# Performance work log

Hardware: AMD Instinct MI355X
Metric: run time of the kernel (lower is better)

Reference implementation:

```python
import jax, jax.numpy as jnp
import numpy as np

S, B, C = 7, 2, 20
LAMBDA_COORD, LAMBDA_NOOBJ = 5.0, 0.5
N, T = 16384, 32


def setup_inputs() -> dict:
    key = jax.random.key(0)
    k1, k2, k3 = jax.random.split(key, 3)
    outputs = jax.random.normal(k1, (N, S, S, B * 5 + C), dtype=jnp.float32)
    # center-format normalized boxes [x, y, w, h] in (0, 1)
    target_boxes = jax.random.uniform(k2, (N, T, 4), dtype=jnp.float32)
    target_labels = jax.random.randint(k3, (N, T), 0, C, dtype=jnp.int32)
    return {"outputs": outputs, "target_boxes": target_boxes, "target_labels": target_labels}


def _iou(b1, b2):
    # center-format boxes [..., 4] -> IoU, broadcasting over leading dims
    x11, y11 = b1[..., 0] - b1[..., 2] / 2, b1[..., 1] - b1[..., 3] / 2
    x12, y12 = b1[..., 0] + b1[..., 2] / 2, b1[..., 1] + b1[..., 3] / 2
    x21, y21 = b2[..., 0] - b2[..., 2] / 2, b2[..., 1] - b2[..., 3] / 2
    x22, y22 = b2[..., 0] + b2[..., 2] / 2, b2[..., 1] + b2[..., 3] / 2
    iw = jnp.clip(jnp.minimum(x12, x22) - jnp.maximum(x11, x21), 0.0)
    ih = jnp.clip(jnp.minimum(y12, y22) - jnp.maximum(y11, y21), 0.0)
    inter = iw * ih
    union = b1[..., 2] * b1[..., 3] + b2[..., 2] * b2[..., 3] - inter
    return inter / jnp.maximum(union, 1e-6)


def yolo_v1_loss(outputs, target_boxes, target_labels):
    n = outputs.shape[0]
    pred_boxes = outputs[..., : B * 4].reshape(n, S, S, B, 4)  # [n,S,S,B,4]
    pred_conf = outputs[..., B * 4 : B * 5]                    # [n,S,S,B]
    pred_cls = outputs[..., B * 5 :]                           # [n,S,S,C]

    cell = 1.0 / S
    g = jnp.arange(S, dtype=jnp.float32)
    px = (pred_boxes[..., 0] + g[None, None, :, None]) * cell  # grid_x varies along dim 2
    py = (pred_boxes[..., 1] + g[None, :, None, None]) * cell  # grid_y varies along dim 1
    pred_boxes_g = jnp.stack([px, py, pred_boxes[..., 2], pred_boxes[..., 3]], axis=-1)

    tx, ty, tw, th = (target_boxes[..., i] for i in range(4))
    gxi = jnp.clip((tx / cell).astype(jnp.int32), 0, S - 1)   # [n,T]
    gyi = jnp.clip((ty / cell).astype(jnp.int32), 0, S - 1)
    ox = (tx - gxi.astype(jnp.float32) * cell) / cell
    oy = (ty - gyi.astype(jnp.float32) * cell) / cell

    bidx = jnp.arange(n)[:, None]
    cell_boxes = pred_boxes_g[bidx, gyi, gxi]  # [n,T,B,4]
    cell_conf = pred_conf[bidx, gyi, gxi]      # [n,T,B]
    cell_cls = pred_cls[bidx, gyi, gxi]        # [n,T,C]

    ious = _iou(target_boxes[:, :, None, :], cell_boxes)          # [n,T,B]
    best = jnp.argmax(ious, axis=-1)                              # [n,T]
    best_box = jnp.take_along_axis(cell_boxes, best[..., None, None], axis=2)[:, :, 0]  # [n,T,4]
    best_conf = jnp.take_along_axis(cell_conf, best[..., None], axis=2)[:, :, 0]        # [n,T]

    pw = jnp.maximum(best_box[..., 2], 1e-6)
    ph = jnp.maximum(best_box[..., 3], 1e-6)
    twc = jnp.maximum(tw, 1e-6)
    thc = jnp.maximum(th, 1e-6)
    box_loss = (
        (best_box[..., 0] - ox) ** 2
        + (best_box[..., 1] - oy) ** 2
        + (jnp.sqrt(pw) - jnp.sqrt(twc)) ** 2
        + (jnp.sqrt(ph) - jnp.sqrt(thc)) ** 2
    ).sum(axis=1)                                                # per-image sum over targets

    obj_loss = ((best_conf - 1.0) ** 2).sum(axis=1)

    onehot = jax.nn.one_hot(target_labels, C, dtype=jnp.float32)
    class_loss = jnp.mean((jax.nn.softmax(cell_cls, axis=-1) - onehot) ** 2, axis=-1).sum(axis=1)

    # obj_mask is never set in the original, so noobj covers every cell/box
    noobj_loss = jnp.mean(pred_conf ** 2, axis=(1, 2, 3))

    per_img = LAMBDA_COORD * box_loss + class_loss + obj_loss + LAMBDA_NOOBJ * noobj_loss
    return jnp.mean(per_img)


def reference(outputs, target_boxes, target_labels):
    return yolo_v1_loss(outputs, target_boxes, target_labels)
```

## Files before the change

kernel.cpp:

```cpp
#include <hip/hip_runtime.h>
#include <math.h>

#define TPB 256
constexpr int kS = 7;
constexpr int kB = 2;
constexpr int kC = 20;
constexpr int kT = 32;
constexpr int kCH = kB * 5 + kC;
constexpr int kCells = kS * kS;
constexpr int kImgF = kCells * kCH;
constexpr int IMGS = 4;

__device__ __forceinline__ float block_reduce(float v, float* red) {
    #pragma unroll
    for (int off = 32; off > 0; off >>= 1)
        v += __shfl_down(v, off, 64);
    const int lane = threadIdx.x & 63;
    const int wave = threadIdx.x >> 6;
    if (lane == 0) red[wave] = v;
    __syncthreads();
    float s = 0.0f;
    if (threadIdx.x == 0) {
        #pragma unroll
        for (int w = 0; w < TPB / 64; w++) s += red[w];
    }
    return s;
}

__global__ __launch_bounds__(TPB) void yolo_stage1(
    const float* __restrict__ outputs,
    const float4* __restrict__ tboxes,
    const int* __restrict__ tlabels,
    float* __restrict__ blocksums,
    int n)
{
    __shared__ float smem[IMGS * kImgF];
    __shared__ float red[TPB / 64];
    const int tid = threadIdx.x;
    const int img0 = blockIdx.x * IMGS;
    const int nimg = min(IMGS, n - img0);

    float local = 0.0f;
    const float kno = 0.5f / (float)(2 * kCells);

    const bool has_tgt = tid < nimg * kT;
    float4 tb = make_float4(0.f, 0.f, 0.f, 0.f);
    int lab = 0;
    if (has_tgt) {
        tb = tboxes[(size_t)img0 * kT + tid];
        lab = tlabels[(size_t)img0 * kT + tid];
    }

    if (nimg == IMGS) {
        const float4* src = reinterpret_cast<const float4*>(outputs + (size_t)img0 * kImgF);
        float4* dst = reinterpret_cast<float4*>(smem);
        constexpr int NV4 = IMGS * kImgF / 4;
        #pragma unroll
        for (int i = 0; i < (NV4 + TPB - 1) / TPB; i++) {
            const int idx = tid + i * TPB;
            if (idx < NV4) {
                const float4 v = src[idx];
                dst[idx] = v;
                const int base = (4 * idx) % 30;
                if (base == 8)      local += kno * (v.x * v.x + v.y * v.y);
                else if (base == 6) local += kno * (v.z * v.z + v.w * v.w);
            }
        }
    } else {
        const float* srcf = outputs + (size_t)img0 * kImgF;
        const int tot = nimg * kImgF;
        for (int i = tid; i < tot; i += TPB) {
            const float v = srcf[i];
            smem[i] = v;
            const int ch = i % kCH;
            if (ch == 8 || ch == 9) local += kno * v * v;
        }
    }
    __syncthreads();

    if (has_tgt) {
        const int sub = tid >> 5;
        const float cellf = 1.0f / 7.0f;
        const float tx = tb.x, ty = tb.y, tw = tb.z, th = tb.w;

        int gxi = (int)(tx / cellf); gxi = min(max(gxi, 0), kS - 1);
        int gyi = (int)(ty / cellf); gyi = min(max(gyi, 0), kS - 1);
        const float ox = (tx - (float)gxi * cellf) / cellf;
        const float oy = (ty - (float)gyi * cellf) / cellf;
        const float* cellp = &smem[sub * kImgF + (gyi * kS + gxi) * kCH];

        const float t_x1 = tx - tw * 0.5f, t_x2 = tx + tw * 0.5f;
        const float t_y1 = ty - th * 0.5f, t_y2 = ty + th * 0.5f;
        const float tarea = tw * th;
        float ious[2], bxs[2], bys[2], bws[2], bhs[2];
        #pragma unroll
        for (int b = 0; b < 2; b++) {
            const float x = cellp[4 * b + 0], y = cellp[4 * b + 1];
            const float w = cellp[4 * b + 2], h = cellp[4 * b + 3];
            const float px = (x + (float)gxi) * cellf;
            const float py = (y + (float)gyi) * cellf;
            const float x21 = px - w * 0.5f, x22 = px + w * 0.5f;
            const float y21 = py - h * 0.5f, y22 = py + h * 0.5f;
            const float iw = fmaxf(fminf(t_x2, x22) - fmaxf(t_x1, x21), 0.0f);
            const float ih = fmaxf(fminf(t_y2, y22) - fmaxf(t_y1, y21), 0.0f);
            const float inter = iw * ih;
            const float uni = tarea + w * h - inter;
            ious[b] = inter / fmaxf(uni, 1e-6f);
            bxs[b] = px; bys[b] = py; bws[b] = w; bhs[b] = h;
        }
        const int best = (ious[1] > ious[0]) ? 1 : 0;

        const float pw = fmaxf(bws[best], 1e-6f), ph = fmaxf(bhs[best], 1e-6f);
        const float twc = fmaxf(tw, 1e-6f), thc = fmaxf(th, 1e-6f);
        const float dx = bxs[best] - ox, dy = bys[best] - oy;
        const float dw = sqrtf(pw) - sqrtf(twc), dh = sqrtf(ph) - sqrtf(thc);
        const float box_loss = dx * dx + dy * dy + dw * dw + dh * dh;

        const float dconf = cellp[8 + best] - 1.0f;
        const float obj_loss = dconf * dconf;

        float m = cellp[10];
        #pragma unroll
        for (int c = 1; c < kC; c++) m = fmaxf(m, cellp[10 + c]);
        float es[kC];
        float ssum = 0.0f;
        #pragma unroll
        for (int c = 0; c < kC; c++) { es[c] = __expf(cellp[10 + c] - m); ssum += es[c]; }
        const float inv = 1.0f / ssum;
        float cl = 0.0f;
        #pragma unroll
        for (int c = 0; c < kC; c++) {
            const float d = es[c] * inv - (c == lab ? 1.0f : 0.0f);
            cl += d * d;
        }

        local += 5.0f * box_loss + obj_loss + cl * (1.0f / (float)kC);
    }

    const float bsum = block_reduce(local, red);
    if (tid == 0) blocksums[blockIdx.x] = bsum;
}

__global__ __launch_bounds__(TPB) void yolo_stage2(
    const float* __restrict__ blocksums, int nblocks, float invn,
    float* __restrict__ out)
{
    __shared__ float red[TPB / 64];
    float local = 0.0f;
    for (int i = threadIdx.x; i < nblocks; i += TPB) local += blocksums[i];
    const float s = block_reduce(local, red);
    if (threadIdx.x == 0) out[0] = s * invn;
}

extern "C" void kernel_launch(void* const* d_in, const int* in_sizes, int n_in,
                              void* d_out, int out_size, void* d_ws, size_t ws_size,
                              hipStream_t stream)
{
    const float* outputs = (const float*)d_in[0];
    const float4* tboxes = (const float4*)d_in[1];
    const int* tlabels = (const int*)d_in[2];
    float* out = (float*)d_out;
    float* blocksums = (float*)d_ws;

    const int n = in_sizes[0] / kImgF;
    const int nblocks = (n + IMGS - 1) / IMGS;

    yolo_stage1<<<nblocks, TPB, 0, stream>>>(outputs, tboxes, tlabels, blocksums, n);
    yolo_stage2<<<1, TPB, 0, stream>>>(blocksums, nblocks, 1.0f / (float)n, out);
}
```

Baseline: 157.8 us.

## Drop LDS staging and gather target cells directly from global memory

Removes the shared-memory copy of each image block and the barrier after it. The streaming pass now only computes the no-object confidence term, and each target thread gathers its cell's 30 values straight from global memory, which should mostly hit cache. Images per block are doubled to 8, and the modulo index is replaced with an incremental counter. This frees LDS and raises occupancy, at the cost of uncoalesced re-reads of cell data from global/L2.

```diff
diff --git a/kernel.cpp b/kernel.cpp
--- a/kernel.cpp
+++ b/kernel.cpp
@@ -9,7 +9,7 @@
 constexpr int kCH = kB * 5 + kC;
 constexpr int kCells = kS * kS;
 constexpr int kImgF = kCells * kCH;
-constexpr int IMGS = 4;
+constexpr int IMGS = 8;
 
 __device__ __forceinline__ float block_reduce(float v, float* red) {
     #pragma unroll
@@ -34,7 +34,6 @@
     float* __restrict__ blocksums,
     int n)
 {
-    __shared__ float smem[IMGS * kImgF];
     __shared__ float red[TPB / 64];
     const int tid = threadIdx.x;
     const int img0 = blockIdx.x * IMGS;
@@ -53,30 +52,31 @@
 
     if (nimg == IMGS) {
         const float4* src = reinterpret_cast<const float4*>(outputs + (size_t)img0 * kImgF);
-        float4* dst = reinterpret_cast<float4*>(smem);
         constexpr int NV4 = IMGS * kImgF / 4;
+        constexpr int FULL = NV4 / TPB;
+        int base = (4 * tid) % 30;
         #pragma unroll
-        for (int i = 0; i < (NV4 + TPB - 1) / TPB; i++) {
-            const int idx = tid + i * TPB;
-            if (idx < NV4) {
-                const float4 v = src[idx];
-                dst[idx] = v;
-                const int base = (4 * idx) % 30;
-                if (base == 8)      local += kno * (v.x * v.x + v.y * v.y);
-                else if (base == 6) local += kno * (v.z * v.z + v.w * v.w);
-            }
+        for (int i = 0; i < FULL; i++) {
+            const float4 v = src[tid + i * TPB];
+            if (base == 8)      local += kno * (v.x * v.x + v.y * v.y);
+            else if (base == 6) local += kno * (v.z * v.z + v.w * v.w);
+            base += 4; if (base >= 30) base -= 30;
+        }
+        const int idx = tid + FULL * TPB;
+        if (idx < NV4) {
+            const float4 v = src[idx];
+            if (base == 8)      local += kno * (v.x * v.x + v.y * v.y);
+            else if (base == 6) local += kno * (v.z * v.z + v.w * v.w);
         }
     } else {
         const float* srcf = outputs + (size_t)img0 * kImgF;
         const int tot = nimg * kImgF;
         for (int i = tid; i < tot; i += TPB) {
             const float v = srcf[i];
-            smem[i] = v;
             const int ch = i % kCH;
             if (ch == 8 || ch == 9) local += kno * v * v;
         }
     }
-    __syncthreads();
 
     if (has_tgt) {
         const int sub = tid >> 5;
@@ -87,7 +87,8 @@
         int gyi = (int)(ty / cellf); gyi = min(max(gyi, 0), kS - 1);
         const float ox = (tx - (float)gxi * cellf) / cellf;
         const float oy = (ty - (float)gyi * cellf) / cellf;
-        const float* cellp = &smem[sub * kImgF + (gyi * kS + gxi) * kCH];
+        const float* __restrict__ cellp =
+            outputs + (size_t)(img0 + sub) * kImgF + (gyi * kS + gxi) * kCH;
 
         const float t_x1 = tx - tw * 0.5f, t_x2 = tx + tw * 0.5f;
         const float t_y1 = ty - th * 0.5f, t_y2 = ty + th * 0.5f;
@@ -119,18 +120,20 @@
         const float dconf = cellp[8 + best] - 1.0f;
         const float obj_loss = dconf * dconf;
 
-        float m = cellp[10];
+        float cls[kC];
         #pragma unroll
-        for (int c = 1; c < kC; c++) m = fmaxf(m, cellp[10 + c]);
-        float es[kC];
+        for (int c = 0; c < kC; c++) cls[c] = cellp[10 + c];
+        float m = cls[0];
+        #pragma unroll
+        for (int c = 1; c < kC; c++) m = fmaxf(m, cls[c]);
         float ssum = 0.0f;
         #pragma unroll
-        for (int c = 0; c < kC; c++) { es[c] = __expf(cellp[10 + c] - m); ssum += es[c]; }
+        for (int c = 0; c < kC; c++) { cls[c] = __expf(cls[c] - m); ssum += cls[c]; }
         const float inv = 1.0f / ssum;
         float cl = 0.0f;
         #pragma unroll
         for (int c = 0; c < kC; c++) {
-            const float d = es[c] * inv - (c == lab ? 1.0f : 0.0f);
+            const float d = cls[c] * inv - (c == lab ? 1.0f : 0.0f);
             cl += d * d;
         }
 
```

Result: slower. 163.2 us (+3.4%).
